# Kernel tuning notes

Hardware: AMD Instinct MI355X
Metric: run time of the kernel (lower is better)

Reference implementation:

```python
import jax, jax.numpy as jnp
import numpy as np

B, DIM, H = 262144, 8, 100


def setup_inputs() -> dict:
    key = jax.random.key(0)
    ks = jax.random.split(key, 11)
    zt1 = jax.random.normal(ks[0], (B, DIM), dtype=jnp.float32)
    zt2 = zt1 + 0.05 * jax.random.normal(ks[1], (B, DIM), dtype=jnp.float32)
    dt = 0.01 * jnp.ones((B,), dtype=jnp.float32)
    s_in = 1.0 / np.sqrt(DIM)
    s_h = 1.0 / np.sqrt(H)
    # drift MLP: Linear(dim,100) -> Softplus -> Linear(100,dim)
    W1m = jax.random.normal(ks[2], (H, DIM), dtype=jnp.float32) * s_in
    b1m = jax.random.normal(ks[3], (H,), dtype=jnp.float32) * s_in
    W2m = jax.random.normal(ks[4], (DIM, H), dtype=jnp.float32) * s_h
    b2m = jax.random.normal(ks[5], (DIM,), dtype=jnp.float32) * s_h
    # diffusion net: Linear(dim,100) -> Softplus -> Linear(100,dim)  (diag=True -> n_entries=dim)
    W1d = jax.random.normal(ks[6], (H, DIM), dtype=jnp.float32) * s_in
    b1d = jax.random.normal(ks[7], (H,), dtype=jnp.float32) * s_in
    W2d = jax.random.normal(ks[8], (DIM, H), dtype=jnp.float32) * s_h
    b2d = jax.random.normal(ks[9], (DIM,), dtype=jnp.float32) * s_h
    return dict(zt1=zt1, zt2=zt2, dt=dt, W1m=W1m, b1m=b1m, W2m=W2m, b2m=b2m,
                W1d=W1d, b1d=b1d, W2d=W2d, b2d=b2d)


def reference(zt1, zt2, dt, W1m, b1m, W2m, b2m, W1d, b1d, W2d, b2d):
    dt0 = dt[0]
    # drift: mu = MLP(zt1) * dt
    mu = jnp.dot(jax.nn.softplus(jnp.dot(zt1, W1m.T) + b1m), W2m.T) + b2m  # [B, dim]
    mu = mu * dt0
    # diffusion: D = exp(Dnet(zt1)); diag Cholesky L = diag(D)
    D = jnp.exp(jnp.dot(jax.nn.softplus(jnp.dot(zt1, W1d.T) + b1d), W2d.T) + b2d)  # [B, dim]
    dz = zt2 - zt1
    # diag=True: cov = diag(D^2), precision = diag(1/D^2), logdet(cov) = 2*sum(log D)
    inv_var = 1.0 / (D * D)
    t1 = 2.0 * jnp.sum(jnp.log(D), axis=-1)
    t2 = jnp.sum(dz * dz * inv_var, axis=-1)
    t3 = -2.0 * jnp.sum(dz * mu * inv_var, axis=-1)
    t4 = jnp.sum(mu * mu * inv_var, axis=-1)
    const = jnp.asarray(-DIM / 2.0 * np.log(2.0 * np.pi), dtype=zt1.dtype)
    log_pz2 = const - 0.5 * (t1 + t2 + t3 + t4)
    loss = jnp.sum(-log_pz2)
    return loss, mu, D * jnp.sqrt(dt0)
```

## Files before the change

### kernel.cpp

```cpp
#include <hip/hip_runtime.h>

constexpr int BN = 262144;
constexpr int H_ = 100;
constexpr int HHALF = 50;
constexpr int RS = 36;

__device__ __forceinline__ float softplus_f(float x) {
    return __logf(1.0f + __expf(x));
}

__global__ __launch_bounds__(256) void pack_w(
    const float* __restrict__ W1m, const float* __restrict__ b1m,
    const float* __restrict__ W2m, const float* __restrict__ W1d,
    const float* __restrict__ b1d, const float* __restrict__ W2d,
    float* __restrict__ rows)
{
    const int gid = blockIdx.x * 256 + threadIdx.x;
    const int NT  = gridDim.x * 256;
    for (int idx = gid; idx < 800; idx += NT) {
        const int j = idx >> 3, k = idx & 7;
        rows[j * RS + 0 + k] = W1m[idx];
        rows[j * RS + 8 + k] = W1d[idx];
    }
    for (int idx = gid; idx < 800; idx += NT) {
        const int k = idx / 100, j = idx - k * 100;
        rows[j * RS + 16 + k] = W2m[idx];
        rows[j * RS + 24 + k] = W2d[idx];
    }
    if (gid < H_) {
        rows[gid * RS + 32] = b1m[gid];
        rows[gid * RS + 33] = b1d[gid];
    }
}

__global__ __launch_bounds__(256) void sde_fused(
    const float* __restrict__ zt1, const float* __restrict__ zt2,
    const float* __restrict__ dtp, const float* __restrict__ b2m,
    const float* __restrict__ b2d, const float* __restrict__ rows,
    float* __restrict__ out)
{
    __shared__ float xch[256 * 9];
    __shared__ float wsum[4];

    const int tid  = threadIdx.x;
    const int lane = tid & 63;
    const int wv   = tid >> 6;
    const int pair = wv >> 1;
    const int h    = __builtin_amdgcn_readfirstlane(wv & 1);
    const int row  = blockIdx.x * 128 + pair * 64 + lane;

    const float dt0  = dtp[0];
    const float sqdt = sqrtf(dt0);

    float x[8];
    {
        const float4* p = reinterpret_cast<const float4*>(zt1) + (size_t)row * 2;
        float4 a = p[0], b = p[1];
        x[0]=a.x; x[1]=a.y; x[2]=a.z; x[3]=a.w;
        x[4]=b.x; x[5]=b.y; x[6]=b.z; x[7]=b.w;
    }
    float4 z2a, z2b;
    {
        const float4* p = reinterpret_cast<const float4*>(zt2) + (size_t)row * 2;
        z2a = p[0]; z2b = p[1];
    }

    float am[8], ad[8];
    if (h == 0) {
        #pragma unroll
        for (int k = 0; k < 8; ++k) { am[k] = b2m[k]; ad[k] = b2d[k]; }
    } else {
        #pragma unroll
        for (int k = 0; k < 8; ++k) { am[k] = 0.f; ad[k] = 0.f; }
    }

    const float* __restrict__ rbase = rows + h * (HHALF * RS);
    #pragma unroll 2
    for (int jj = 0; jj < HHALF; ++jj) {
        const float* r = rbase + jj * RS;
        float pm = r[32], pd = r[33];
        #pragma unroll
        for (int k = 0; k < 8; ++k) {
            pm = fmaf(x[k], r[k],     pm);
            pd = fmaf(x[k], r[8 + k], pd);
        }
        const float hm = softplus_f(pm);
        const float hd = softplus_f(pd);
        #pragma unroll
        for (int k = 0; k < 8; ++k) {
            am[k] = fmaf(hm, r[16 + k], am[k]);
            ad[k] = fmaf(hd, r[24 + k], ad[k]);
        }
    }

    float* mine = &xch[tid * 9];
    if (h == 0) {
        mine[0]=am[4]; mine[1]=am[5]; mine[2]=am[6]; mine[3]=am[7];
        mine[4]=ad[4]; mine[5]=ad[5]; mine[6]=ad[6]; mine[7]=ad[7];
    } else {
        mine[0]=am[0]; mine[1]=am[1]; mine[2]=am[2]; mine[3]=am[3];
        mine[4]=ad[0]; mine[5]=ad[1]; mine[6]=ad[2]; mine[7]=ad[3];
    }
    __syncthreads();
    const float* part = &xch[(tid ^ 64) * 9];

    float* __restrict__ mu_out = out + 1;
    float* __restrict__ sg_out = out + 1 + (size_t)BN * 8;

    float t1 = 0.f, t2 = 0.f, t3 = 0.f, t4 = 0.f;

#define EPI(K0, ZB)                                                          \
    {                                                                        \
        const float z2v[4] = {ZB.x, ZB.y, ZB.z, ZB.w};                       \
        _Pragma("unroll")                                                    \
        for (int q = 0; q < 4; ++q) {                                        \
            const int k = K0 + q;                                            \
            const float a_m = am[k] + part[q];                               \
            const float a_d = ad[k] + part[4 + q];                           \
            const float mu = a_m * dt0;                                      \
            const float y  = a_d;                        \
            const float Dk = __expf(y);                                      \
            const float iv = __expf(-2.0f * y);                   \
            const float dz = z2v[q] - x[k];                                  \
            t1 += y;                                                         \
            t2 = fmaf(dz * dz, iv, t2);                                      \
            t3 = fmaf(dz * mu, iv, t3);                                      \
            t4 = fmaf(mu * mu, iv, t4);                                      \
            mu_out[(size_t)row * 8 + k] = mu;                                \
            sg_out[(size_t)row * 8 + k] = Dk * sqdt;                         \
        }                                                                    \
    }

    if (h == 0) { EPI(0, z2a) } else { EPI(4, z2b) }
#undef EPI

    float nll = fmaf(0.5f, (2.0f * t1 + t2 - 2.0f * t3 + t4),
                     3.67575413281869039f);

    #pragma unroll
    for (int off = 32; off > 0; off >>= 1) nll += __shfl_down(nll, off);

    if (lane == 0) wsum[wv] = nll;
    __syncthreads();
    if (tid == 0) atomicAdd(out, wsum[0] + wsum[1] + wsum[2] + wsum[3]);
}

extern "C" void kernel_launch(void* const* d_in, const int* in_sizes, int n_in,
                              void* d_out, int out_size, void* d_ws, size_t ws_size,
                              hipStream_t stream) {
    float* rows = (float*)d_ws;
    hipMemsetAsync(d_out, 0, sizeof(float), stream);
    pack_w<<<4, 256, 0, stream>>>(
        (const float*)d_in[3], (const float*)d_in[4],
        (const float*)d_in[5],
        (const float*)d_in[7], (const float*)d_in[8],
        (const float*)d_in[9],
        rows);
    sde_fused<<<BN / 128, 256, 0, stream>>>(
        (const float*)d_in[0], (const float*)d_in[1], (const float*)d_in[2],
        (const float*)d_in[6], (const float*)d_in[10],
        rows, (float*)d_out);
}
```

Before: 138.8 us.

## Fold log2e/ln2 into packed weights and use packed v2f FMAs

Prescales the first-layer weights and biases by log2(e) and the second-layer weights by ln2 when packing, so softplus can be computed with base-2 exp/log and no extra multiplies per hidden unit. The inner MLP loops are rewritten with 2-wide vector FMAs, which can map to packed FP32 instructions on CDNA. This halves the FMA instruction count in the hot loop but adds horizontal adds for the first-layer dot products and changes the summation order slightly.

```diff
diff --git a/kernel.cpp b/kernel.cpp
--- a/kernel.cpp
+++ b/kernel.cpp
@@ -5,9 +5,7 @@
 constexpr int HHALF = 50;
 constexpr int RS = 36;
 
-__device__ __forceinline__ float softplus_f(float x) {
-    return __logf(1.0f + __expf(x));
-}
+typedef float v2f __attribute__((ext_vector_type(2)));
 
 __global__ __launch_bounds__(256) void pack_w(
     const float* __restrict__ W1m, const float* __restrict__ b1m,
@@ -15,21 +13,23 @@
     const float* __restrict__ b1d, const float* __restrict__ W2d,
     float* __restrict__ rows)
 {
+    constexpr float LOG2E = 1.4426950408889634f;
+    constexpr float LN2   = 0.6931471805599453f;
     const int gid = blockIdx.x * 256 + threadIdx.x;
     const int NT  = gridDim.x * 256;
     for (int idx = gid; idx < 800; idx += NT) {
         const int j = idx >> 3, k = idx & 7;
-        rows[j * RS + 0 + k] = W1m[idx];
-        rows[j * RS + 8 + k] = W1d[idx];
+        rows[j * RS + 0 + k] = W1m[idx] * LOG2E;
+        rows[j * RS + 8 + k] = W1d[idx] * LOG2E;
     }
     for (int idx = gid; idx < 800; idx += NT) {
         const int k = idx / 100, j = idx - k * 100;
-        rows[j * RS + 16 + k] = W2m[idx];
-        rows[j * RS + 24 + k] = W2d[idx];
+        rows[j * RS + 16 + k] = W2m[idx] * LN2;
+        rows[j * RS + 24 + k] = W2d[idx] * LN2;
     }
     if (gid < H_) {
-        rows[gid * RS + 32] = b1m[gid];
-        rows[gid * RS + 33] = b1d[gid];
+        rows[gid * RS + 32] = b1m[gid] * LOG2E;
+        rows[gid * RS + 33] = b1d[gid] * LOG2E;
     }
 }
 
@@ -52,12 +52,15 @@
     const float dt0  = dtp[0];
     const float sqdt = sqrtf(dt0);
 
+    v2f xv[4];
     float x[8];
     {
         const float4* p = reinterpret_cast<const float4*>(zt1) + (size_t)row * 2;
         float4 a = p[0], b = p[1];
         x[0]=a.x; x[1]=a.y; x[2]=a.z; x[3]=a.w;
         x[4]=b.x; x[5]=b.y; x[6]=b.z; x[7]=b.w;
+        xv[0] = (v2f){a.x, a.y}; xv[1] = (v2f){a.z, a.w};
+        xv[2] = (v2f){b.x, b.y}; xv[3] = (v2f){b.z, b.w};
     }
     float4 z2a, z2b;
     {
@@ -65,41 +68,49 @@
         z2a = p[0]; z2b = p[1];
     }
 
-    float am[8], ad[8];
+    v2f amv[4], adv[4];
     if (h == 0) {
         #pragma unroll
-        for (int k = 0; k < 8; ++k) { am[k] = b2m[k]; ad[k] = b2d[k]; }
+        for (int q = 0; q < 4; ++q) {
+            amv[q] = (v2f){b2m[2*q], b2m[2*q+1]};
+            adv[q] = (v2f){b2d[2*q], b2d[2*q+1]};
+        }
     } else {
         #pragma unroll
-        for (int k = 0; k < 8; ++k) { am[k] = 0.f; ad[k] = 0.f; }
+        for (int q = 0; q < 4; ++q) { amv[q] = (v2f){0.f, 0.f}; adv[q] = (v2f){0.f, 0.f}; }
     }
 
     const float* __restrict__ rbase = rows + h * (HHALF * RS);
     #pragma unroll 2
     for (int jj = 0; jj < HHALF; ++jj) {
         const float* r = rbase + jj * RS;
-        float pm = r[32], pd = r[33];
+        const v2f* rv = reinterpret_cast<const v2f*>(r);
+        v2f pmv = (v2f){0.f, 0.f}, pdv = (v2f){0.f, 0.f};
         #pragma unroll
-        for (int k = 0; k < 8; ++k) {
-            pm = fmaf(x[k], r[k],     pm);
-            pd = fmaf(x[k], r[8 + k], pd);
+        for (int q = 0; q < 4; ++q) {
+            pmv = __builtin_elementwise_fma(xv[q], rv[q],     pmv);
+            pdv = __builtin_elementwise_fma(xv[q], rv[4 + q], pdv);
         }
-        const float hm = softplus_f(pm);
-        const float hd = softplus_f(pd);
+        const float pm = (pmv.x + pmv.y) + r[32];
+        const float pd = (pdv.x + pdv.y) + r[33];
+        const float hm = log2f(1.0f + exp2f(pm));
+        const float hd = log2f(1.0f + exp2f(pd));
+        const v2f hm2 = (v2f){hm, hm};
+        const v2f hd2 = (v2f){hd, hd};
         #pragma unroll
-        for (int k = 0; k < 8; ++k) {
-            am[k] = fmaf(hm, r[16 + k], am[k]);
-            ad[k] = fmaf(hd, r[24 + k], ad[k]);
+        for (int q = 0; q < 4; ++q) {
+            amv[q] = __builtin_elementwise_fma(hm2, rv[8 + q],  amv[q]);
+            adv[q] = __builtin_elementwise_fma(hd2, rv[12 + q], adv[q]);
         }
     }
 
     float* mine = &xch[tid * 9];
     if (h == 0) {
-        mine[0]=am[4]; mine[1]=am[5]; mine[2]=am[6]; mine[3]=am[7];
-        mine[4]=ad[4]; mine[5]=ad[5]; mine[6]=ad[6]; mine[7]=ad[7];
+        mine[0]=amv[2].x; mine[1]=amv[2].y; mine[2]=amv[3].x; mine[3]=amv[3].y;
+        mine[4]=adv[2].x; mine[5]=adv[2].y; mine[6]=adv[3].x; mine[7]=adv[3].y;
     } else {
-        mine[0]=am[0]; mine[1]=am[1]; mine[2]=am[2]; mine[3]=am[3];
-        mine[4]=ad[0]; mine[5]=ad[1]; mine[6]=ad[2]; mine[7]=ad[3];
+        mine[0]=amv[0].x; mine[1]=amv[0].y; mine[2]=amv[1].x; mine[3]=amv[1].y;
+        mine[4]=adv[0].x; mine[5]=adv[0].y; mine[6]=adv[1].x; mine[7]=adv[1].y;
     }
     __syncthreads();
     const float* part = &xch[(tid ^ 64) * 9];
@@ -109,14 +120,16 @@
 
     float t1 = 0.f, t2 = 0.f, t3 = 0.f, t4 = 0.f;
 
-#define EPI(K0, ZB)                                                          \
+#define EPI(K0, A0, A1, D0, D1, ZB)                                          \
     {                                                                        \
+        const float amk[4] = {A0.x, A0.y, A1.x, A1.y};                       \
+        const float adk[4] = {D0.x, D0.y, D1.x, D1.y};                       \
         const float z2v[4] = {ZB.x, ZB.y, ZB.z, ZB.w};                       \
         _Pragma("unroll")                                                    \
         for (int q = 0; q < 4; ++q) {                                        \
             const int k = K0 + q;                                            \
-            const float a_m = am[k] + part[q];                               \
-            const float a_d = ad[k] + part[4 + q];                           \
+            const float a_m = amk[q] + part[q];                              \
+            const float a_d = adk[q] + part[4 + q];                          \
             const float mu = a_m * dt0;                                      \
             const float y  = a_d;                        \
             const float Dk = __expf(y);                                      \
@@ -131,7 +144,8 @@
         }                                                                    \
     }
 
-    if (h == 0) { EPI(0, z2a) } else { EPI(4, z2b) }
+    if (h == 0) { EPI(0, amv[0], amv[1], adv[0], adv[1], z2a) }
+    else        { EPI(4, amv[2], amv[3], adv[2], adv[3], z2b) }
 #undef EPI
 
     float nll = fmaf(0.5f, (2.0f * t1 + t2 - 2.0f * t3 + t4),
```

Result: faster. 135.3 us (-2.5%).
